# Kernel optimization log

Hardware: AMD Instinct MI355X
Metric: run time of the kernel (lower is better)

The kernel has to match this reference:

```python
import jax, jax.numpy as jnp
import numpy as np

N = 100000      # nodes
E = 1600000     # edges
F = 92          # raw node feature length
H = 128         # element_embedding == hidden_encoding (GatedGraphConv out_channels)
STEPS = 6       # mpnn_steps
G = 256         # graphs in batch


def setup_inputs() -> dict:
    key = jax.random.key(0)
    ks = jax.random.split(key, 10)
    s = 0.05
    x = jax.random.normal(ks[0], (N, F), dtype=jnp.float32)
    edge_index = jax.random.randint(ks[1], (2, E), 0, N, dtype=jnp.int64)
    batch = jnp.sort(jax.random.randint(ks[2], (N,), 0, G, dtype=jnp.int64))
    # atom_input: Linear(F, H, bias=False); applied as x @ W_embed with W_embed [F, H]
    W_embed = jax.random.normal(ks[3], (F, H), dtype=jnp.float32) * s
    # GatedGraphConv weight: [num_layers, H, H], used as h @ W_mpnn[i]
    W_mpnn = jax.random.normal(ks[4], (STEPS, H, H), dtype=jnp.float32) * s
    # torch.nn.GRUCell params: weight_ih/hh [3H, H], bias_ih/hh [3H]
    w_ih = jax.random.normal(ks[5], (3 * H, H), dtype=jnp.float32) * s
    w_hh = jax.random.normal(ks[6], (3 * H, H), dtype=jnp.float32) * s
    b_ih = jax.random.normal(ks[7], (3 * H,), dtype=jnp.float32) * s
    b_hh = jax.random.normal(ks[8], (3 * H,), dtype=jnp.float32) * s
    # prediction_layer: Linear(H, 1)
    w_pred = jax.random.normal(ks[9], (H, 1), dtype=jnp.float32) * s
    b_pred = jnp.zeros((1,), dtype=jnp.float32)
    return {"x": x, "edge_index": edge_index, "batch": batch,
            "W_embed": W_embed, "W_mpnn": W_mpnn,
            "w_ih": w_ih, "w_hh": w_hh, "b_ih": b_ih, "b_hh": b_hh,
            "w_pred": w_pred, "b_pred": b_pred}


def reference(x, edge_index, batch, W_embed, W_mpnn, w_ih, w_hh, b_ih, b_hh, w_pred, b_pred):
    n = x.shape[0]
    src, dst = edge_index[0], edge_index[1]  # PyG: messages flow source -> target
    # atom_input (no bias) + tanh; element_embedding == H so no zero-padding needed
    h = jnp.tanh(x @ W_embed)  # [N, H]

    def step(h, W):
        m = h @ W                                             # per-step linear [N, H]
        agg = jax.ops.segment_sum(m[src], dst, num_segments=n)  # scatter-add aggr
        # torch GRUCell(input=agg, hidden=h)
        gi = agg @ w_ih.T + b_ih                              # [N, 3H]
        gh = h @ w_hh.T + b_hh                                # [N, 3H]
        i_r, i_z, i_n = jnp.split(gi, 3, axis=-1)
        h_r, h_z, h_n = jnp.split(gh, 3, axis=-1)
        r = jax.nn.sigmoid(i_r + h_r)
        z = jax.nn.sigmoid(i_z + h_z)
        cand = jnp.tanh(i_n + r * h_n)
        h_new = (1.0 - z) * cand + z * h
        return h_new, None

    h, _ = jax.lax.scan(step, h, W_mpnn)

    # global_mean_pool over graph ids
    sums = jax.ops.segment_sum(h, batch, num_segments=G)                           # [G, H]
    counts = jax.ops.segment_sum(jnp.ones((n, 1), h.dtype), batch, num_segments=G)  # [G, 1]
    pooled = sums / jnp.maximum(counts, 1.0)
    pooled = jax.nn.relu(pooled)
    return (pooled @ w_pred + b_pred)[:, 0]  # [G]
```

## Files before the change

### kernel.cpp

```cpp
#include <hip/hip_runtime.h>
#include <math.h>

#define N_NODES 100000
#define N_PAD   100032
#define N_EDGES 1600000
#define F_IN    92
#define H_DIM   128
#define STEPS   6
#define G_GRAPHS 256
#define TH3     384
#define SSTR    136
#define HSTR    132
#define FPASS   8
#define FRANGE  12500

typedef __attribute__((ext_vector_type(8))) short bf16x8;
typedef __attribute__((ext_vector_type(4))) float f32x4;

__device__ __forceinline__ unsigned short f2bf(float x) {
    unsigned u = __float_as_uint(x);
    return (unsigned short)((u + 0x7fffu + ((u >> 16) & 1u)) >> 16);
}
__device__ __forceinline__ float bf2f(unsigned short h) {
    return __uint_as_float(((unsigned)h) << 16);
}

__global__ void fuse_w_kernel(const float* __restrict__ Wm, const float* __restrict__ w_ih,
                              float* __restrict__ M2) {
    int ij = blockIdx.x;
    int i  = ij / TH3;
    int j  = ij - i * TH3;
    int k  = threadIdx.x;
    __shared__ float wj[H_DIM];
    wj[k] = w_ih[j * H_DIM + k];
    __syncthreads();
    const float* wr = Wm + ((size_t)i * H_DIM + k) * H_DIM;
    float acc = 0.f;
    #pragma unroll 4
    for (int c = 0; c < H_DIM; ++c) acc = fmaf(wj[c], wr[c], acc);
    M2[((size_t)i * TH3 + j) * H_DIM + k] = acc;
}

__global__ void pack_kernel(const float* __restrict__ M6, const float* __restrict__ w_hh,
                            unsigned short* __restrict__ PBhi, unsigned short* __restrict__ PBlo) {
    int b    = blockIdx.x;
    int lane = threadIdx.x;
    int kc   = b & 3;
    int ct   = (b >> 2) & 7;
    int mg   = b >> 5;
    int g    = mg % 3;
    int mat  = mg / 3;
    int j    = g * 128 + ct * 16 + (lane & 15);
    int k0   = kc * 32 + (lane >> 4) * 8;
    size_t outBase = ((size_t)b * 64 + lane) * 8;
    #pragma unroll
    for (int jj = 0; jj < 8; ++jj) {
        int k = k0 + jj;
        float v = (mat < 6) ? M6[((size_t)mat * TH3 + j) * H_DIM + k]
                            : w_hh[(size_t)j * H_DIM + k];
        unsigned short hv = f2bf(v);
        PBhi[outBase + jj] = hv;
        PBlo[outBase + jj] = f2bf(v - bf2f(hv));
    }
}

#define ET 16
__global__ void embed_kernel(const float* __restrict__ x, const float* __restrict__ We,
                             unsigned short* __restrict__ h_hi, unsigned short* __restrict__ h_lo) {
    int n0 = blockIdx.x * ET;
    int j  = threadIdx.x;
    __shared__ float xs[ET * F_IN];
    for (int i = j; i < ET * F_IN; i += H_DIM) xs[i] = x[n0 * F_IN + i];
    __syncthreads();
    float acc[ET];
    #pragma unroll
    for (int n = 0; n < ET; ++n) acc[n] = 0.f;
    const float4* xs4 = (const float4*)xs;
    for (int k4 = 0; k4 < F_IN / 4; ++k4) {
        int k = k4 * 4;
        float w0 = We[(k + 0) * H_DIM + j];
        float w1 = We[(k + 1) * H_DIM + j];
        float w2 = We[(k + 2) * H_DIM + j];
        float w3 = We[(k + 3) * H_DIM + j];
        #pragma unroll
        for (int n = 0; n < ET; ++n) {
            float4 a = xs4[n * (F_IN / 4) + k4];
            acc[n] = fmaf(a.x, w0, acc[n]);
            acc[n] = fmaf(a.y, w1, acc[n]);
            acc[n] = fmaf(a.z, w2, acc[n]);
            acc[n] = fmaf(a.w, w3, acc[n]);
        }
    }
    #pragma unroll
    for (int n = 0; n < ET; ++n) {
        float e2 = __expf(2.f * acc[n]);
        float v  = 1.f - 2.f / (e2 + 1.f);
        size_t o = (size_t)(n0 + n) * H_DIM + j;
        unsigned short hv = f2bf(v);
        h_hi[o] = hv;
        h_lo[o] = f2bf(v - bf2f(hv));
    }
}

__global__ void hist_kernel(const int* __restrict__ dst, int* __restrict__ count) {
    int e = blockIdx.x * 256 + threadIdx.x;
    if (e < N_EDGES) atomicAdd(&count[dst[e]], 1);
}

__global__ void scan_block_kernel(const int* __restrict__ count, int* __restrict__ offs,
                                  int* __restrict__ blockSums) {
    __shared__ int tmp[256];
    int i = blockIdx.x * 256 + threadIdx.x;
    int t = threadIdx.x;
    int v = (i < N_NODES) ? count[i] : 0;
    tmp[t] = v;
    __syncthreads();
    for (int d = 1; d < 256; d <<= 1) {
        int add = (t >= d) ? tmp[t - d] : 0;
        __syncthreads();
        tmp[t] += add;
        __syncthreads();
    }
    if (i < N_NODES) offs[i] = tmp[t] - v;
    if (t == 255) blockSums[blockIdx.x] = tmp[255];
}

__global__ void scan_sums_kernel(int* __restrict__ blockSums, int nb) {
    __shared__ int tmp[512];
    int t = threadIdx.x;
    int v = (t < nb) ? blockSums[t] : 0;
    tmp[t] = v;
    __syncthreads();
    for (int d = 1; d < 512; d <<= 1) {
        int add = (t >= d) ? tmp[t - d] : 0;
        __syncthreads();
        tmp[t] += add;
        __syncthreads();
    }
    if (t < nb) blockSums[t] = tmp[t] - v;
}

__global__ void scan_add_kernel(int* __restrict__ offs, const int* __restrict__ blockSums) {
    int i = blockIdx.x * 256 + threadIdx.x;
    if (i < N_NODES) offs[i] += blockSums[blockIdx.x];
    if (i == 0) offs[N_NODES] = N_EDGES;
}

__global__ void fill_kernel(const int* __restrict__ src, const int* __restrict__ dst,
                            const int* __restrict__ offs, int* __restrict__ cursor,
                            int* __restrict__ srcSorted) {
    int e = blockIdx.x * 256 + threadIdx.x;
    if (e >= N_EDGES) return;
    for (int p = 0; p < FPASS; ++p) {
        int lo = p * FRANGE;
        int d = dst[e];
        if (d >= lo && d < lo + FRANGE) {
            int pos = atomicAdd(&cursor[d], 1);
            srcSorted[offs[d] + pos] = src[e];
        }
    }
}

__global__ __launch_bounds__(512, 4) void gru_fused_kernel(
    const unsigned short* __restrict__ h_hi_in,
    unsigned short* __restrict__ h_hi_out,
    unsigned short* __restrict__ h_lo,
    const int* __restrict__ offs, const int* __restrict__ srcS,
    const unsigned short* __restrict__ PBhi, const unsigned short* __restrict__ PBlo,
    int matI, const float* __restrict__ b_ih, const float* __restrict__ b_hh)
{
    __shared__ __align__(16) unsigned short buf[3 * 32 * SSTR];
    unsigned short* sHh = buf;
    unsigned short* sHl = buf + 32 * SSTR;
    unsigned short* sS  = buf + 2 * 32 * SSTR;
    float* hnF = (float*)buf;

    int nt = blockIdx.x;
    int rowBase = nt * 32;
    int t = threadIdx.x;
    int row = t >> 4;
    int c8  = (t & 15) * 8;

    {
        size_t g = (size_t)(rowBase + row) * H_DIM + c8;
        int l = row * SSTR + c8;
        *(bf16x8*)&sHh[l] = *(const bf16x8*)(h_hi_in + g);
        *(bf16x8*)&sHl[l] = *(const bf16x8*)(h_lo + g);
    }
    __syncthreads();

    {
        float a[8];
        #pragma unroll
        for (int j = 0; j < 8; ++j) a[j] = 0.f;
        int node = rowBase + row;
        if (node < N_NODES) {
            int beg = offs[node], end = offs[node + 1];
            int i = beg;
            for (; i + 4 <= end; i += 4) {
                int n0 = srcS[i], n1 = srcS[i + 1], n2 = srcS[i + 2], n3 = srcS[i + 3];
                bf16x8 v0 = *(const bf16x8*)(h_hi_in + (size_t)n0 * H_DIM + c8);
                bf16x8 v1 = *(const bf16x8*)(h_hi_in + (size_t)n1 * H_DIM + c8);
                bf16x8 v2 = *(const bf16x8*)(h_hi_in + (size_t)n2 * H_DIM + c8);
                bf16x8 v3 = *(const bf16x8*)(h_hi_in + (size_t)n3 * H_DIM + c8);
                #pragma unroll
                for (int j = 0; j < 8; ++j)
                    a[j] += (bf2f((unsigned short)v0[j]) + bf2f((unsigned short)v1[j]))
                          + (bf2f((unsigned short)v2[j]) + bf2f((unsigned short)v3[j]));
            }
            if (i + 2 <= end) {
                int n0 = srcS[i], n1 = srcS[i + 1];
                bf16x8 v0 = *(const bf16x8*)(h_hi_in + (size_t)n0 * H_DIM + c8);
                bf16x8 v1 = *(const bf16x8*)(h_hi_in + (size_t)n1 * H_DIM + c8);
                #pragma unroll
                for (int j = 0; j < 8; ++j)
                    a[j] += bf2f((unsigned short)v0[j]) + bf2f((unsigned short)v1[j]);
                i += 2;
            }
            if (i < end) {
                int n0 = srcS[i];
                bf16x8 v0 = *(const bf16x8*)(h_hi_in + (size_t)n0 * H_DIM + c8);
                #pragma unroll
                for (int j = 0; j < 8; ++j) a[j] += bf2f((unsigned short)v0[j]);
            }
        }
        bf16x8 o;
        #pragma unroll
        for (int j = 0; j < 8; ++j) o[j] = (short)f2bf(a[j]);
        *(bf16x8*)&sS[row * SSTR + c8] = o;
    }

    int lane = t & 63;
    int ct   = t >> 6;
    int rloc = lane & 15;
    int kOff = (lane >> 4) * 8;

    f32x4 accRZ[2][2], accIn[2], accHn[2];
    #pragma unroll
    for (int rs = 0; rs < 2; ++rs) {
        accRZ[0][rs] = (f32x4){0.f, 0.f, 0.f, 0.f};
        accRZ[1][rs] = (f32x4){0.f, 0.f, 0.f, 0.f};
        accIn[rs]    = (f32x4){0.f, 0.f, 0.f, 0.f};
        accHn[rs]    = (f32x4){0.f, 0.f, 0.f, 0.f};
    }

    for (int kc = 0; kc < 4; ++kc) {
        int aOff = kc * 32 + kOff;
        bf16x8 aHh4[2], aHl4[2];
        #pragma unroll
        for (int rs = 0; rs < 2; ++rs) {
            int al = (rs * 16 + rloc) * SSTR + aOff;
            aHh4[rs] = *(const bf16x8*)(&sHh[al]);
            aHl4[rs] = *(const bf16x8*)(&sHl[al]);
        }
        #pragma unroll
        for (int g = 0; g < 3; ++g) {
            size_t oH = ((size_t)((18 + g) * 32 + ct * 4 + kc) * 64 + lane) * 8;
            bf16x8 bHh = *(const bf16x8*)(PBhi + oH);
            bf16x8 bHl = *(const bf16x8*)(PBlo + oH);
            #pragma unroll
            for (int rs = 0; rs < 2; ++rs) {
                f32x4* tH = (g == 0) ? &accRZ[0][rs] : (g == 1) ? &accRZ[1][rs] : &accHn[rs];
                *tH = __builtin_amdgcn_mfma_f32_16x16x32_bf16(aHh4[rs], bHh, *tH, 0, 0, 0);
                *tH = __builtin_amdgcn_mfma_f32_16x16x32_bf16(aHl4[rs], bHh, *tH, 0, 0, 0);
                *tH = __builtin_amdgcn_mfma_f32_16x16x32_bf16(aHh4[rs], bHl, *tH, 0, 0, 0);
            }
        }
    }

    __syncthreads();

    const int fI0 = matI * 3;
    for (int kc = 0; kc < 4; ++kc) {
        int aOff = kc * 32 + kOff;
        bf16x8 aS[2];
        #pragma unroll
        for (int rs = 0; rs < 2; ++rs)
            aS[rs] = *(const bf16x8*)(&sS[(rs * 16 + rloc) * SSTR + aOff]);
        #pragma unroll
        for (int g = 0; g < 3; ++g) {
            size_t oI = ((size_t)((fI0 + g) * 32 + ct * 4 + kc) * 64 + lane) * 8;
            bf16x8 bIh = *(const bf16x8*)(PBhi + oI);
            bf16x8 bIl = *(const bf16x8*)(PBlo + oI);
            #pragma unroll
            for (int rs = 0; rs < 2; ++rs) {
                f32x4* tI = (g == 0) ? &accRZ[0][rs] : (g == 1) ? &accRZ[1][rs] : &accIn[rs];
                *tI = __builtin_amdgcn_mfma_f32_16x16x32_bf16(aS[rs], bIh, *tI, 0, 0, 0);
                *tI = __builtin_amdgcn_mfma_f32_16x16x32_bf16(aS[rs], bIl, *tI, 0, 0, 0);
            }
        }
    }

    int c = ct * 16 + rloc;
    float br  = b_ih[c] + b_hh[c];
    float bz  = b_ih[128 + c] + b_hh[128 + c];
    float bin = b_ih[256 + c], bhn = b_hh[256 + c];
    int rl = (lane >> 4) * 4;

    float hnv[2][4];
    #pragma unroll
    for (int rs = 0; rs < 2; ++rs) {
        #pragma unroll
        for (int r = 0; r < 4; ++r) {
            int lrow = rs * 16 + rl + r;
            float hold = bf2f(sHh[lrow * SSTR + c]) + bf2f(sHl[lrow * SSTR + c]);
            float rr = 1.f / (1.f + __expf(-(accRZ[0][rs][r] + br)));
            float zz = 1.f / (1.f + __expf(-(accRZ[1][rs][r] + bz)));
            float pre = (accIn[rs][r] + bin) + rr * (accHn[rs][r] + bhn);
            float e2 = __expf(2.f * pre);
            float cand = 1.f - 2.f / (e2 + 1.f);
            hnv[rs][r] = (1.f - zz) * cand + zz * hold;
        }
    }
    __syncthreads();
    #pragma unroll
    for (int rs = 0; rs < 2; ++rs)
        #pragma unroll
        for (int r = 0; r < 4; ++r)
            hnF[(rs * 16 + rl + r) * HSTR + c] = hnv[rs][r];
    __syncthreads();
    #pragma unroll
    for (int i = t; i < 32 * 32; i += 512) {
        int rw = i >> 5;
        int c4 = (i & 31) * 4;
        int gRow = rowBase + rw;
        if (gRow < N_NODES) {
            float4 v = *(const float4*)(&hnF[rw * HSTR + c4]);
            ushort4 hh, ll;
            hh.x = f2bf(v.x); ll.x = f2bf(v.x - bf2f(hh.x));
            hh.y = f2bf(v.y); ll.y = f2bf(v.y - bf2f(hh.y));
            hh.z = f2bf(v.z); ll.z = f2bf(v.z - bf2f(hh.z));
            hh.w = f2bf(v.w); ll.w = f2bf(v.w - bf2f(hh.w));
            size_t o = (size_t)gRow * H_DIM + c4;
            *(ushort4*)(h_hi_out + o) = hh;
            *(ushort4*)(h_lo + o) = ll;
        }
    }
}

__global__ void pool_partial(const unsigned short* __restrict__ h_hi,
                             const unsigned short* __restrict__ h_lo,
                             const int* __restrict__ batch,
                             float* __restrict__ pooled) {
    int b = blockIdx.x;
    int t = threadIdx.x;
    int n0 = b * 64;
    if (n0 >= N_NODES) return;
    int nEnd = n0 + 64 < N_NODES ? n0 + 64 : N_NODES;
    int curG = batch[n0];
    float acc = 0.f;
    for (int n = n0; n < nEnd; ++n) {
        int g = batch[n];
        if (g != curG) {
            atomicAdd(&pooled[curG * H_DIM + t], acc);
            acc = 0.f;
            curG = g;
        }
        size_t o = (size_t)n * H_DIM + t;
        acc += bf2f(h_hi[o]) + bf2f(h_lo[o]);
    }
    atomicAdd(&pooled[curG * H_DIM + t], acc);
}

__global__ void pool_head(const float* __restrict__ pooled, const int* __restrict__ batch,
                          const float* __restrict__ w_pred, const float* __restrict__ b_pred,
                          float* __restrict__ out) {
    int g = blockIdx.x;
    int t = threadIdx.x;
    __shared__ int bounds[2];
    __shared__ float red[2];
    if (t < 2) {
        int target = g + t;
        int lo = 0, hi = N_NODES;
        while (lo < hi) {
            int mid = (lo + hi) >> 1;
            if (batch[mid] < target) lo = mid + 1; else hi = mid;
        }
        bounds[t] = lo;
    }
    __syncthreads();
    int cnt = bounds[1] - bounds[0];
    float pv = pooled[g * H_DIM + t] / fmaxf((float)cnt, 1.f);
    pv = fmaxf(pv, 0.f);
    float v = pv * w_pred[t];
    #pragma unroll
    for (int off = 32; off > 0; off >>= 1) v += __shfl_down(v, off);
    if ((t & 63) == 0) red[t >> 6] = v;
    __syncthreads();
    if (t == 0) out[g] = red[0] + red[1] + b_pred[0];
}

extern "C" void kernel_launch(void* const* d_in, const int* in_sizes, int n_in,
                              void* d_out, int out_size, void* d_ws, size_t ws_size,
                              hipStream_t stream) {
    const float* x      = (const float*)d_in[0];
    const int*   ei     = (const int*)d_in[1];
    const int*   batch  = (const int*)d_in[2];
    const float* We     = (const float*)d_in[3];
    const float* Wm     = (const float*)d_in[4];
    const float* w_ih   = (const float*)d_in[5];
    const float* w_hh   = (const float*)d_in[6];
    const float* b_ih   = (const float*)d_in[7];
    const float* b_hh   = (const float*)d_in[8];
    const float* w_pred = (const float*)d_in[9];
    const float* b_pred = (const float*)d_in[10];
    float* out = (float*)d_out;

    const size_t HN = (size_t)N_PAD * H_DIM;
    unsigned short* h_hiA = (unsigned short*)d_ws;
    unsigned short* h_lo  = h_hiA + HN;
    unsigned short* h_hiB = h_lo + HN;
    float* M6 = (float*)(h_hiB + HN);
    unsigned short* PBhi = (unsigned short*)(M6 + (size_t)STEPS * TH3 * H_DIM);
    unsigned short* PBlo = PBhi + 21 * 32 * 64 * 8;
    int* offs      = (int*)(PBlo + 21 * 32 * 64 * 8);
    int* srcSorted = offs + (N_NODES + 1);
    float* pooled  = (float*)(srcSorted + N_EDGES);
    int* count     = (int*)h_hiB;
    int* cursor    = count + N_NODES;
    int* blockSums = cursor + N_NODES;

    const int* esrc = ei;
    const int* edst = ei + N_EDGES;
    const int EB = (N_EDGES + 255) / 256;
    const int NB = (N_NODES + 255) / 256;

    hipMemsetAsync(count, 0, 2 * (size_t)N_NODES * sizeof(int), stream);
    hipMemsetAsync(pooled, 0, (size_t)G_GRAPHS * H_DIM * sizeof(float), stream);
    hist_kernel<<<EB, 256, 0, stream>>>(edst, count);
    scan_block_kernel<<<NB, 256, 0, stream>>>(count, offs, blockSums);
    scan_sums_kernel<<<1, 512, 0, stream>>>(blockSums, NB);
    scan_add_kernel<<<NB, 256, 0, stream>>>(offs, blockSums);
    fill_kernel<<<EB, 256, 0, stream>>>(esrc, edst, offs, cursor, srcSorted);

    fuse_w_kernel<<<STEPS * TH3, H_DIM, 0, stream>>>(Wm, w_ih, M6);
    pack_kernel<<<21 * 32, 64, 0, stream>>>(M6, w_hh, PBhi, PBlo);
    embed_kernel<<<N_NODES / ET, H_DIM, 0, stream>>>(x, We, h_hiA, h_lo);

    for (int i = 0; i < STEPS; ++i) {
        const unsigned short* hin = (i & 1) ? h_hiB : h_hiA;
        unsigned short*       hout = (i & 1) ? h_hiA : h_hiB;
        gru_fused_kernel<<<N_PAD / 32, 512, 0, stream>>>(hin, hout, h_lo,
                                                         offs, srcSorted, PBhi, PBlo,
                                                         i, b_ih, b_hh);
    }

    pool_partial<<<(N_NODES + 63) / 64, H_DIM, 0, stream>>>(h_hiA, h_lo, batch, pooled);
    pool_head<<<G_GRAPHS, H_DIM, 0, stream>>>(pooled, batch, w_pred, b_pred, out);
}
```

Before: 1.107 ms.

## Balance edge gather across threads with edge-range strips and LDS atomics

The neighbor gather now splits the 32-row tile's whole edge range evenly into 64 strips of 8 threads. Each thread handles 16 columns, walks its strip across row boundaries, and flushes partial sums into a float LDS accumulator with atomicAdd. The goal is to remove the load imbalance that comes from varying node degrees, where one 16-thread group per row serialized on high-degree nodes. The cost is extra LDS use (a separate float buffer), shared-memory atomics, and zero-initialization. One barrier is dropped because hnF no longer aliases the tile buffer.

```diff
diff --git a/kernel.cpp b/kernel.cpp
--- a/kernel.cpp
+++ b/kernel.cpp
@@ -170,63 +170,83 @@
     int matI, const float* __restrict__ b_ih, const float* __restrict__ b_hh)
 {
     __shared__ __align__(16) unsigned short buf[3 * 32 * SSTR];
+    __shared__ __align__(16) float sSf[32 * HSTR];
+    __shared__ int offsL[33];
     unsigned short* sHh = buf;
     unsigned short* sHl = buf + 32 * SSTR;
     unsigned short* sS  = buf + 2 * 32 * SSTR;
-    float* hnF = (float*)buf;
+    float* hnF = sSf;
 
     int nt = blockIdx.x;
     int rowBase = nt * 32;
     int t = threadIdx.x;
     int row = t >> 4;
-    int c8  = (t & 15) * 8;
 
     {
+        int c8 = (t & 15) * 8;
         size_t g = (size_t)(rowBase + row) * H_DIM + c8;
         int l = row * SSTR + c8;
         *(bf16x8*)&sHh[l] = *(const bf16x8*)(h_hi_in + g);
         *(bf16x8*)&sHl[l] = *(const bf16x8*)(h_lo + g);
     }
+    #pragma unroll
+    for (int i = t; i < 32 * HSTR; i += 512) sSf[i] = 0.f;
+    if (t < 33) {
+        int nn = rowBase + t;
+        offsL[t] = offs[nn < N_NODES ? nn : N_NODES];
+    }
     __syncthreads();
 
     {
-        float a[8];
-        #pragma unroll
-        for (int j = 0; j < 8; ++j) a[j] = 0.f;
-        int node = rowBase + row;
-        if (node < N_NODES) {
-            int beg = offs[node], end = offs[node + 1];
-            int i = beg;
-            for (; i + 4 <= end; i += 4) {
-                int n0 = srcS[i], n1 = srcS[i + 1], n2 = srcS[i + 2], n3 = srcS[i + 3];
-                bf16x8 v0 = *(const bf16x8*)(h_hi_in + (size_t)n0 * H_DIM + c8);
-                bf16x8 v1 = *(const bf16x8*)(h_hi_in + (size_t)n1 * H_DIM + c8);
-                bf16x8 v2 = *(const bf16x8*)(h_hi_in + (size_t)n2 * H_DIM + c8);
-                bf16x8 v3 = *(const bf16x8*)(h_hi_in + (size_t)n3 * H_DIM + c8);
+        int eBeg  = offsL[0], eEnd = offsL[32];
+        int total = eEnd - eBeg;
+        int chunk = t & 7;
+        int strip = t >> 3;
+        int q = total >> 6, rem = total & 63;
+        int s0 = eBeg + strip * q + (strip < rem ? strip : rem);
+        int s1 = s0 + q + (strip < rem ? 1 : 0);
+        int cOff = chunk * 16;
+        if (s1 > s0) {
+            float a[16];
+            #pragma unroll
+            for (int j = 0; j < 16; ++j) a[j] = 0.f;
+            int r = 0;
+            #pragma unroll
+            for (int stp = 16; stp > 0; stp >>= 1)
+                if (r + stp <= 31 && offsL[r + stp] <= s0) r += stp;
+            int rNext = offsL[r + 1];
+            const unsigned short* hb = h_hi_in + cOff;
+            int i = s0;
+            while (i < s1) {
+                int stop = rNext < s1 ? rNext : s1;
+                for (; i < stop; ++i) {
+                    int n = srcS[i];
+                    const bf16x8* p = (const bf16x8*)(hb + (size_t)n * H_DIM);
+                    bf16x8 va = p[0], vb = p[1];
+                    #pragma unroll
+                    for (int j = 0; j < 8; ++j) {
+                        a[j]     += bf2f((unsigned short)va[j]);
+                        a[8 + j] += bf2f((unsigned short)vb[j]);
+                    }
+                }
                 #pragma unroll
-                for (int j = 0; j < 8; ++j)
-                    a[j] += (bf2f((unsigned short)v0[j]) + bf2f((unsigned short)v1[j]))
-                          + (bf2f((unsigned short)v2[j]) + bf2f((unsigned short)v3[j]));
+                for (int j = 0; j < 16; ++j) {
+                    atomicAdd(&sSf[r * HSTR + cOff + j], a[j]);
+                    a[j] = 0.f;
+                }
+                if (i < s1) {
+                    do { ++r; rNext = offsL[r + 1]; } while (rNext <= i);
+                }
             }
-            if (i + 2 <= end) {
-                int n0 = srcS[i], n1 = srcS[i + 1];
-                bf16x8 v0 = *(const bf16x8*)(h_hi_in + (size_t)n0 * H_DIM + c8);
-                bf16x8 v1 = *(const bf16x8*)(h_hi_in + (size_t)n1 * H_DIM + c8);
-                #pragma unroll
-                for (int j = 0; j < 8; ++j)
-                    a[j] += bf2f((unsigned short)v0[j]) + bf2f((unsigned short)v1[j]);
-                i += 2;
-            }
-            if (i < end) {
-                int n0 = srcS[i];
-                bf16x8 v0 = *(const bf16x8*)(h_hi_in + (size_t)n0 * H_DIM + c8);
-                #pragma unroll
-                for (int j = 0; j < 8; ++j) a[j] += bf2f((unsigned short)v0[j]);
-            }
-        }
+        }
+    }
+    __syncthreads();
+
+    {
+        int c8 = (t & 15) * 8;
         bf16x8 o;
         #pragma unroll
-        for (int j = 0; j < 8; ++j) o[j] = (short)f2bf(a[j]);
+        for (int j = 0; j < 8; ++j) o[j] = (short)f2bf(sSf[row * HSTR + c8 + j]);
         *(bf16x8*)&sS[row * SSTR + c8] = o;
     }
 
@@ -312,7 +332,6 @@
             hnv[rs][r] = (1.f - zz) * cand + zz * hold;
         }
     }
-    __syncthreads();
     #pragma unroll
     for (int rs = 0; rs < 2; ++rs)
         #pragma unroll
```

Result: slower. 2.055 ms (+85.7%).
